# Performance work log

Measured on AMD Instinct MI355X. Metric: run time of the kernel, lower is better.

## Reference

```python
import jax, jax.numpy as jnp
import numpy as np

J, L = 4, 8
M = N = 128
B = 2
EPS = 1e-6  # abs_eps smoothing: |z|_eps = sqrt(re^2 + im^2 + eps)


def indices_third_order(J, L):
    # For each bandpass filter i = j1*L + l1, pair with every filter of scale
    # j2 >= j1 (all L angles) plus the lowpass (index J*L).
    # Count = J*L*(L*(J+1)/2 + 1) == num_coefficients.
    i_list, j_list = [], []
    for j1 in range(J):
        for l1 in range(L):
            i = j1 * L + l1
            for j2 in range(j1, J):
                for l2 in range(L):
                    i_list.append(i)
                    j_list.append(j2 * L + l2)
            i_list.append(i)
            j_list.append(J * L)
    return np.asarray(i_list), np.asarray(j_list)


def make_filters(J, L, M, N):
    # Real frequency-domain Morlet-like Gaussian bumps at J scales x L angles,
    # plus one lowpass. Shape (1, J*L+1, M, N), float32.
    kx = 2.0 * np.pi * np.fft.fftfreq(M)[:, None]
    ky = 2.0 * np.pi * np.fft.fftfreq(N)[None, :]
    filts = []
    for j in range(J):
        k0 = 0.8 * np.pi / 2.0 ** j
        sigma = 0.5 * k0
        for l in range(L):
            theta = np.pi * l / L
            cx, cy = k0 * np.cos(theta), k0 * np.sin(theta)
            filts.append(np.exp(-((kx - cx) ** 2 + (ky - cy) ** 2) / (2.0 * sigma ** 2)))
    sigma_lp = 0.8 * np.pi / 2.0 ** J
    filts.append(np.exp(-(kx ** 2 + ky ** 2) / (2.0 * sigma_lp ** 2)))
    return np.stack(filts)[None].astype(np.float32)


def abs_eps(z):
    return jnp.sqrt(z.real ** 2 + z.imag ** 2 + EPS)


def setup_inputs() -> dict:
    key = jax.random.key(0)
    x = jax.random.normal(key, (B, 1, M, N), dtype=jnp.float32)
    filters = jnp.asarray(make_filters(J, L, M, N))  # (1, 33, M, N)
    return {"x": x, "filters": filters}


def reference(x, filters):
    idx0, idx1 = indices_third_order(J, L)
    # first-order filtering: (B, nf, M, N) complex
    xf = jnp.fft.ifft2(filters * jnp.fft.fft2(x))
    xa = abs_eps(xf)  # real (B, nf, M, N)
    # cross-scale correlation: (B, nf_i, nf_j, M, N)
    inner = jnp.fft.ifft2(filters[:, None] * jnp.fft.fft2(xa)[:, :, None])
    out = jnp.real(jnp.conj(xf)[:, None] * inner).mean(axis=(-2, -1))  # (B, nf, nf)
    return out[:, idx0, idx1]  # (B, 672)
```

## Files before the change

kernel.cpp:

```cpp
#include <hip/hip_runtime.h>
#include <math.h>


#define PI_F 3.14159265358979323846f

__device__ __forceinline__ void make_tw(int lane, float* twr, float* twi) {
#pragma unroll
  for (int s = 0; s < 6; ++s) {
    int h = 32 >> s;
    float ang = -PI_F * (float)(lane & (h - 1)) / (float)h;
    float sv, cv;
    __sincosf(ang, &sv, &cv);
    twr[s] = cv; twi[s] = sv;
  }
  float ang = -PI_F * (float)lane / 64.0f;
  float sv, cv;
  __sincosf(ang, &sv, &cv);
  twr[6] = cv; twi[6] = sv;
}

template <int S>
__device__ __forceinline__ void fft128_dif(float& ar, float& ai, float& br, float& bi,
                                           const float* twr, const float* twi, int lane) {
  float s6r = twr[6], s6i = (S > 0) ? twi[6] : -twi[6];
  float ur = ar + br, ui = ai + bi;
  float vr = ar - br, vi = ai - bi;
  ar = ur; ai = ui;
  br = vr * s6r - vi * s6i;
  bi = vr * s6i + vi * s6r;
#pragma unroll
  for (int s = 0; s < 6; ++s) {
    int h = 32 >> s;
    float wr = twr[s], wi = (S > 0) ? twi[s] : -twi[s];
    bool hi = (lane & h) != 0;
    float pr, pi2;
    pr = __shfl_xor(ar, h, 64); pi2 = __shfl_xor(ai, h, 64);
    if (!hi) { ar += pr; ai += pi2; }
    else { float dr = pr - ar, di = pi2 - ai; ar = dr * wr - di * wi; ai = dr * wi + di * wr; }
    pr = __shfl_xor(br, h, 64); pi2 = __shfl_xor(bi, h, 64);
    if (!hi) { br += pr; bi += pi2; }
    else { float dr = pr - br, di = pi2 - bi; br = dr * wr - di * wi; bi = dr * wi + di * wr; }
  }
}

__device__ __forceinline__ void transpose_r2c(float (&dr)[16], float (&di)[16],
    float (&er)[8], float (&ei)[8], float (&fr)[8], float (&fi2)[8],
    float2 (*tile)[128], int lane, int w) {
#pragma unroll
  for (int ch = 0; ch < 2; ++ch) {
    if ((w >> 3) == ch) {
#pragma unroll
      for (int t = 0; t < 8; ++t) {
        int r = w * 8 + t;
        int rr = r & 63, sw = r & 15;
        tile[rr][lane ^ sw] = make_float2(dr[2 * t], di[2 * t]);
        tile[rr][(lane + 64) ^ sw] = make_float2(dr[2 * t + 1], di[2 * t + 1]);
      }
    }
    __syncthreads();
    {
      int sw = lane & 15;
#pragma unroll
      for (int ci = 0; ci < 8; ++ci) {
        int c = w * 8 + ci;
        float2 v = tile[lane][c ^ sw];
        if (ch == 0) { er[ci] = v.x; ei[ci] = v.y; }
        else { fr[ci] = v.x; fi2[ci] = v.y; }
      }
    }
    __syncthreads();
  }
}

__global__ __launch_bounds__(1024, 2) void k_prep(const float* __restrict__ x,
    float2* __restrict__ X, float* __restrict__ out) {
  __shared__ float2 tile[64][128];
  int tid = threadIdx.x;
  if (blockIdx.x == 2) {
    if (tid < 1344) out[tid] = 0.f;
    if (tid < 320) out[tid + 1024] = 0.f;
    return;
  }
  int b = blockIdx.x;
  int lane = tid & 63, w = tid >> 6;
  float twr[7], twi[7]; make_tw(lane, twr, twi);
  const float* xb = x + b * 16384;
  float dr[16], di[16];
  float er[8], ei[8], fr[8], fi2[8];
#pragma unroll
  for (int t = 0; t < 8; ++t) {
    int r = w * 8 + t;
    float ar = xb[r * 128 + lane], ai2 = 0.f, br = xb[r * 128 + lane + 64], bi = 0.f;
    fft128_dif<1>(ar, ai2, br, bi, twr, twi, lane);
    dr[2 * t] = ar; di[2 * t] = ai2; dr[2 * t + 1] = br; di[2 * t + 1] = bi;
  }
  transpose_r2c(dr, di, er, ei, fr, fi2, tile, lane, w);
  int u0 = __brev((unsigned)lane) >> 25;
#pragma unroll
  for (int ci = 0; ci < 8; ++ci) {
    int c = w * 8 + ci;
    float ar = er[ci], ai2 = ei[ci], br = fr[ci], bi = fi2[ci];
    fft128_dif<1>(ar, ai2, br, bi, twr, twi, lane);
    int vn = __brev((unsigned)c) >> 25;
    X[b * 16384 + u0 * 128 + vn] = make_float2(ar, ai2);
    X[b * 16384 + (u0 + 1) * 128 + vn] = make_float2(br, bi);
  }
}

__global__ __launch_bounds__(1024, 2) void k_fields(const float2* __restrict__ X,
    const float* __restrict__ F, float* __restrict__ dfld, float* __restrict__ xa) {
  __shared__ float2 tile[64][128];
  int tid = threadIdx.x, lane = tid & 63, w = tid >> 6;
  bool isd = (blockIdx.x < 66);
  int b, f;
  float* optr;
  if (isd) {
    b = blockIdx.x / 33; f = blockIdx.x - b * 33;
    optr = dfld + blockIdx.x * 16384;
  } else {
    int q = blockIdx.x - 66; b = q >> 5; f = q & 31;
    optr = xa + q * 16384;
  }
  const float* Fb = F + f * 16384;
  float twr[7], twi[7]; make_tw(lane, twr, twi);
  const float2* Xb = X + b * 16384;
  float dr[16], di[16];
  float er[8], ei[8], fr[8], fi2[8];

#pragma unroll
  for (int t = 0; t < 8; ++t) {
    int r = w * 8 + t;
    float2 x0 = Xb[r * 128 + lane];
    float2 x1 = Xb[r * 128 + lane + 64];
    float f0 = Fb[r * 128 + lane], f1 = Fb[r * 128 + lane + 64];
    if (isd) { f0 *= f0; f1 *= f1; }
    float ar = x0.x * f0, ai2 = x0.y * f0, br = x1.x * f1, bi = x1.y * f1;
    fft128_dif<-1>(ar, ai2, br, bi, twr, twi, lane);
    dr[2 * t] = ar; di[2 * t] = ai2; dr[2 * t + 1] = br; di[2 * t + 1] = bi;
  }
  transpose_r2c(dr, di, er, ei, fr, fi2, tile, lane, w);

  const float sc = 1.0f / 16384.0f;
#pragma unroll
  for (int ci = 0; ci < 8; ++ci) {
    int c = w * 8 + ci;
    float ar = er[ci], ai2 = ei[ci], br = fr[ci], bi = fi2[ci];
    fft128_dif<-1>(ar, ai2, br, bi, twr, twi, lane);
    if (isd) {
      optr[c * 128 + lane] = ar;
      optr[c * 128 + lane + 64] = br;
    } else {
      float t0r = ar * sc, t0i = ai2 * sc, t1r = br * sc, t1i = bi * sc;
      optr[c * 128 + lane] = sqrtf(t0r * t0r + t0i * t0i + 1e-6f);
      optr[c * 128 + lane + 64] = sqrtf(t1r * t1r + t1i * t1i + 1e-6f);
    }
  }
}

__global__ __launch_bounds__(512) void k_dot(const float* __restrict__ xa,
    const float* __restrict__ dfld, float* __restrict__ out) {
  int im = blockIdx.x >> 2;
  int slice = blockIdx.x & 3;
  int b = im >> 5, i = im & 31;
  int t = threadIdx.x;
  const float4* xr = (const float4*)(xa + im * 16384 + slice * 4096);
  const float4* db = (const float4*)(dfld + b * 33 * 16384 + slice * 4096);
  float acc[33];
#pragma unroll
  for (int j = 0; j < 33; ++j) acc[j] = 0.f;
#pragma unroll
  for (int it = 0; it < 2; ++it) {
    int k = it * 512 + t;
    float4 xv = xr[k];
#pragma unroll
    for (int j = 0; j < 33; ++j) {
      float4 dv = db[j * 4096 + k];
      acc[j] += xv.x * dv.x + xv.y * dv.y + xv.z * dv.z + xv.w * dv.w;
    }
  }
#pragma unroll
  for (int j = 0; j < 33; ++j) {
#pragma unroll
    for (int off = 32; off > 0; off >>= 1) acc[j] += __shfl_xor(acc[j], off, 64);
  }
  __shared__ float red[8][33];
  int w = t >> 6, lane = t & 63;
  if (lane == 0) {
#pragma unroll
    for (int j = 0; j < 33; ++j) red[w][j] = acc[j];
  }
  __syncthreads();
  if (t < 33) {
    float s = 0.f;
#pragma unroll
    for (int w2 = 0; w2 < 8; ++w2) s += red[w2][t];
    int j = t;
    int j1 = i >> 3, l1 = i & 7;
    const int pref[4] = {0, 264, 464, 600};
    int per = (4 - j1) * 8 + 1;
    int start = pref[j1] + l1 * per;
    int pos = -1;
    if (j == 32) pos = start + per - 1;
    else {
      int j2 = j >> 3;
      if (j2 >= j1) pos = start + (j2 - j1) * 8 + (j & 7);
    }
    if (pos >= 0)
      atomicAdd(out + b * 672 + pos, s * (1.0f / 16384.0f) * (1.0f / 16384.0f));
  }
}

extern "C" void kernel_launch(void* const* d_in, const int* in_sizes, int n_in,
                              void* d_out, int out_size, void* d_ws, size_t ws_size,
                              hipStream_t stream) {
  (void)in_sizes; (void)n_in; (void)out_size; (void)ws_size;
  const float* x = (const float*)d_in[0];
  const float* F = (const float*)d_in[1];
  float* out = (float*)d_out;
  char* ws = (char*)d_ws;
  float2* X = (float2*)(ws + 0);
  float* dfld = (float*)(ws + 262144);
  float* xa = (float*)(ws + 4587520);

  hipLaunchKernelGGL(k_prep, dim3(3), dim3(1024), 0, stream, x, X, out);
  hipLaunchKernelGGL(k_fields, dim3(130), dim3(1024), 0, stream, X, F, dfld, xa);
  hipLaunchKernelGGL(k_dot, dim3(256), dim3(512), 0, stream, xa, dfld, out);
}
```

Measured before the change: 113.7 us.

## Pack two real-output inverse FFTs per complex transform and split column passes across blocks

Precomputes Hermitian-symmetrized squared filters G = (F^2 + F(-k)^2)/2 so that each d-field inverse FFT gives a real output. Two such fields are packed as the real and imaginary parts of one complex IFFT, which halves the d-field transform work. Both k_prep and k_fields now split the column FFT pass into two half-blocks to raise the block count. In exchange, the row FFT pass is computed redundantly in each half-block, and G costs an extra pass over the filters every call plus extra workspace.

```diff
diff --git a/kernel.cpp b/kernel.cpp
--- a/kernel.cpp
+++ b/kernel.cpp
@@ -43,9 +43,9 @@
   }
 }
 
-__device__ __forceinline__ void transpose_r2c(float (&dr)[16], float (&di)[16],
-    float (&er)[8], float (&ei)[8], float (&fr)[8], float (&fi2)[8],
-    float2 (*tile)[128], int lane, int w) {
+__device__ __forceinline__ void transpose_r2c_half(float (&dr)[16], float (&di)[16],
+    float (&er)[4], float (&ei)[4], float (&fr)[4], float (&fi2)[4],
+    float2 (*tile)[128], int lane, int w, int colbase) {
 #pragma unroll
   for (int ch = 0; ch < 2; ++ch) {
     if ((w >> 3) == ch) {
@@ -61,8 +61,8 @@
     {
       int sw = lane & 15;
 #pragma unroll
-      for (int ci = 0; ci < 8; ++ci) {
-        int c = w * 8 + ci;
+      for (int ci = 0; ci < 4; ++ci) {
+        int c = colbase + w * 4 + ci;
         float2 v = tile[lane][c ^ sw];
         if (ch == 0) { er[ci] = v.x; ei[ci] = v.y; }
         else { fr[ci] = v.x; fi2[ci] = v.y; }
@@ -73,20 +73,33 @@
 }
 
 __global__ __launch_bounds__(1024, 2) void k_prep(const float* __restrict__ x,
-    float2* __restrict__ X, float* __restrict__ out) {
+    float2* __restrict__ X, float* __restrict__ out, const float* __restrict__ F,
+    float* __restrict__ G) {
   __shared__ float2 tile[64][128];
   int tid = threadIdx.x;
-  if (blockIdx.x == 2) {
+  int bx = blockIdx.x;
+  if (bx == 4) {
     if (tid < 1344) out[tid] = 0.f;
-    if (tid < 320) out[tid + 1024] = 0.f;
     return;
   }
-  int b = blockIdx.x;
+  if (bx >= 5) {
+    int j = bx - 5;
+    const float* Fj = F + j * 16384;
+    float* Gj = G + j * 16384;
+    for (int k = tid; k < 16384; k += 1024) {
+      int u = k >> 7, v = k & 127;
+      int un = (128 - u) & 127, vn = (128 - v) & 127;
+      float f = Fj[k], fn = Fj[un * 128 + vn];
+      Gj[k] = 0.5f * (f * f + fn * fn);
+    }
+    return;
+  }
+  int b = bx >> 1, half = bx & 1;
   int lane = tid & 63, w = tid >> 6;
   float twr[7], twi[7]; make_tw(lane, twr, twi);
   const float* xb = x + b * 16384;
   float dr[16], di[16];
-  float er[8], ei[8], fr[8], fi2[8];
+  float er[4], ei[4], fr[4], fi2[4];
 #pragma unroll
   for (int t = 0; t < 8; ++t) {
     int r = w * 8 + t;
@@ -94,11 +107,11 @@
     fft128_dif<1>(ar, ai2, br, bi, twr, twi, lane);
     dr[2 * t] = ar; di[2 * t] = ai2; dr[2 * t + 1] = br; di[2 * t + 1] = bi;
   }
-  transpose_r2c(dr, di, er, ei, fr, fi2, tile, lane, w);
+  transpose_r2c_half(dr, di, er, ei, fr, fi2, tile, lane, w, half * 64);
   int u0 = __brev((unsigned)lane) >> 25;
 #pragma unroll
-  for (int ci = 0; ci < 8; ++ci) {
-    int c = w * 8 + ci;
+  for (int ci = 0; ci < 4; ++ci) {
+    int c = half * 64 + w * 4 + ci;
     float ar = er[ci], ai2 = ei[ci], br = fr[ci], bi = fi2[ci];
     fft128_dif<1>(ar, ai2, br, bi, twr, twi, lane);
     int vn = __brev((unsigned)c) >> 25;
@@ -108,51 +121,74 @@
 }
 
 __global__ __launch_bounds__(1024, 2) void k_fields(const float2* __restrict__ X,
-    const float* __restrict__ F, float* __restrict__ dfld, float* __restrict__ xa) {
+    const float* __restrict__ F, const float* __restrict__ G,
+    float* __restrict__ dfld, float* __restrict__ xa) {
   __shared__ float2 tile[64][128];
   int tid = threadIdx.x, lane = tid & 63, w = tid >> 6;
-  bool isd = (blockIdx.x < 66);
-  int b, f;
-  float* optr;
+  int bx = blockIdx.x;
+  bool isd = (bx < 68);
+  int b, half;
+  bool has1 = false;
+  const float* g0 = nullptr; const float* g1 = nullptr; const float* Fb = nullptr;
+  float* o0; float* o1 = nullptr;
   if (isd) {
-    b = blockIdx.x / 33; f = blockIdx.x - b * 33;
-    optr = dfld + blockIdx.x * 16384;
+    int dp = bx >> 1; half = bx & 1;
+    b = dp / 17; int p = dp - b * 17;
+    int j0 = 2 * p; has1 = (p < 16);
+    g0 = G + j0 * 16384;
+    g1 = G + (j0 + 1) * 16384;
+    o0 = dfld + (b * 33 + j0) * 16384;
+    o1 = dfld + (b * 33 + j0 + 1) * 16384;
   } else {
-    int q = blockIdx.x - 66; b = q >> 5; f = q & 31;
-    optr = xa + q * 16384;
-  }
-  const float* Fb = F + f * 16384;
+    int q = bx - 68; int qi = q >> 1; half = q & 1;
+    b = qi >> 5; int f = qi & 31;
+    Fb = F + f * 16384;
+    o0 = xa + qi * 16384;
+  }
   float twr[7], twi[7]; make_tw(lane, twr, twi);
   const float2* Xb = X + b * 16384;
   float dr[16], di[16];
-  float er[8], ei[8], fr[8], fi2[8];
+  float er[4], ei[4], fr[4], fi2[4];
 
 #pragma unroll
   for (int t = 0; t < 8; ++t) {
     int r = w * 8 + t;
     float2 x0 = Xb[r * 128 + lane];
     float2 x1 = Xb[r * 128 + lane + 64];
-    float f0 = Fb[r * 128 + lane], f1 = Fb[r * 128 + lane + 64];
-    if (isd) { f0 *= f0; f1 *= f1; }
-    float ar = x0.x * f0, ai2 = x0.y * f0, br = x1.x * f1, bi = x1.y * f1;
+    float ar, ai2, br, bi;
+    if (isd) {
+      float ga = g0[r * 128 + lane];
+      float gb = has1 ? g1[r * 128 + lane] : 0.f;
+      float gc = g0[r * 128 + lane + 64];
+      float gd = has1 ? g1[r * 128 + lane + 64] : 0.f;
+      ar = x0.x * ga - x0.y * gb; ai2 = x0.y * ga + x0.x * gb;
+      br = x1.x * gc - x1.y * gd; bi = x1.y * gc + x1.x * gd;
+    } else {
+      float f0 = Fb[r * 128 + lane], f1 = Fb[r * 128 + lane + 64];
+      ar = x0.x * f0; ai2 = x0.y * f0; br = x1.x * f1; bi = x1.y * f1;
+    }
     fft128_dif<-1>(ar, ai2, br, bi, twr, twi, lane);
     dr[2 * t] = ar; di[2 * t] = ai2; dr[2 * t + 1] = br; di[2 * t + 1] = bi;
   }
-  transpose_r2c(dr, di, er, ei, fr, fi2, tile, lane, w);
+  transpose_r2c_half(dr, di, er, ei, fr, fi2, tile, lane, w, half * 64);
 
   const float sc = 1.0f / 16384.0f;
 #pragma unroll
-  for (int ci = 0; ci < 8; ++ci) {
-    int c = w * 8 + ci;
+  for (int ci = 0; ci < 4; ++ci) {
+    int c = half * 64 + w * 4 + ci;
     float ar = er[ci], ai2 = ei[ci], br = fr[ci], bi = fi2[ci];
     fft128_dif<-1>(ar, ai2, br, bi, twr, twi, lane);
     if (isd) {
-      optr[c * 128 + lane] = ar;
-      optr[c * 128 + lane + 64] = br;
+      o0[c * 128 + lane] = ar;
+      o0[c * 128 + lane + 64] = br;
+      if (has1) {
+        o1[c * 128 + lane] = ai2;
+        o1[c * 128 + lane + 64] = bi;
+      }
     } else {
       float t0r = ar * sc, t0i = ai2 * sc, t1r = br * sc, t1i = bi * sc;
-      optr[c * 128 + lane] = sqrtf(t0r * t0r + t0i * t0i + 1e-6f);
-      optr[c * 128 + lane + 64] = sqrtf(t1r * t1r + t1i * t1i + 1e-6f);
+      o0[c * 128 + lane] = sqrtf(t0r * t0r + t0i * t0i + 1e-6f);
+      o0[c * 128 + lane + 64] = sqrtf(t1r * t1r + t1i * t1i + 1e-6f);
     }
   }
 }
@@ -221,8 +257,9 @@
   float2* X = (float2*)(ws + 0);
   float* dfld = (float*)(ws + 262144);
   float* xa = (float*)(ws + 4587520);
-
-  hipLaunchKernelGGL(k_prep, dim3(3), dim3(1024), 0, stream, x, X, out);
-  hipLaunchKernelGGL(k_fields, dim3(130), dim3(1024), 0, stream, X, F, dfld, xa);
+  float* G = (float*)(ws + 8781824);
+
+  hipLaunchKernelGGL(k_prep, dim3(38), dim3(1024), 0, stream, x, X, out, F, G);
+  hipLaunchKernelGGL(k_fields, dim3(196), dim3(1024), 0, stream, X, F, G, dfld, xa);
   hipLaunchKernelGGL(k_dot, dim3(256), dim3(512), 0, stream, xa, dfld, out);
 }
```

Result: faster. 106.1 us (-6.7%).
